# Performance work log

Measured on AMD Instinct MI355X. Metric: run time of the kernel, lower is better.

## Reference

```python
import jax, jax.numpy as jnp
import numpy as np

DIM = 256
NUM_HEADS = 8
HEAD_DIM = DIM // NUM_HEADS


def setup_inputs() -> dict:
    key = jax.random.key(0)
    k1, k2, k3, k4 = jax.random.split(key, 4)
    B, C, H, W = 16, DIM, 64, 64
    x = jax.random.normal(k1, (B, C, H, W), dtype=jnp.float32)
    # 1x1 convs as dense weight matrices [out_ch, in_ch]
    Wqkv = jax.random.normal(k2, (3 * DIM, DIM), dtype=jnp.float32) * (DIM ** -0.5)
    Wproj = jax.random.normal(k3, (DIM, DIM), dtype=jnp.float32) * (DIM ** -0.5)
    bproj = jax.random.normal(k4, (DIM,), dtype=jnp.float32) * 0.01
    return {"x": x, "Wqkv": Wqkv, "Wproj": Wproj, "bproj": bproj}


def reference(x, Wqkv, Wproj, bproj):
    B, C, H, W = x.shape
    N = H * W
    hd = C // NUM_HEADS

    # qkv: 1x1 conv (no bias) == channel matmul
    qkv = jnp.einsum('oc,bchw->bohw', Wqkv, x)  # [B, 3C, H, W]
    q, k, v = jnp.split(qkv, 3, axis=1)

    def to_heads(t):
        # b (h d) x y -> b h (x y) d
        return t.reshape(B, NUM_HEADS, hd, N).transpose(0, 1, 3, 2)

    q, k, v = to_heads(q), to_heads(k), to_heads(v)  # [B, h, N, d]

    # linear attention feature map + per-token normalization over d
    q = jax.nn.elu(q) + 1.0
    k = jax.nn.elu(k) + 1.0
    q = q / jnp.sum(q, axis=-1, keepdims=True)
    k = k / jnp.sum(k, axis=-1, keepdims=True)

    kv = jnp.einsum('bhnd,bhne->bhde', k, v)   # [B, h, d, d]
    out = jnp.einsum('bhnd,bhde->bhne', q, kv)  # [B, h, N, d]

    # b h (x y) d -> b (h d) x y
    out = out.transpose(0, 1, 3, 2).reshape(B, C, H, W)

    # proj: 1x1 conv with bias; drop_path is identity in eval mode
    out = jnp.einsum('oc,bchw->bohw', Wproj, out) + bproj[None, :, None, None]
    return out + x
```

## Files before the change

kernel.cpp:

```cpp
#include <hip/hip_runtime.h>
#include <stdint.h>
#include <stddef.h>

#define DIM   256
#define NH    8
#define HD    32
#define BATCH 16
#define NTOK  4096

typedef __attribute__((ext_vector_type(8))) short short8;
typedef __attribute__((ext_vector_type(4))) float f32x4;

__device__ __forceinline__ unsigned short f2bf(float x){
  unsigned u = __float_as_uint(x);
  u += 0x7fffu + ((u >> 16) & 1u);
  return (unsigned short)(u >> 16);
}
__device__ __forceinline__ float elu1(float v){
  return (v > 0.f) ? (v + 1.f) : __expf(v);
}
__device__ __forceinline__ void gload_lds16(const void* g, void* lds){
  __builtin_amdgcn_global_load_lds(
      (const __attribute__((address_space(1))) unsigned int*)g,
      (__attribute__((address_space(3))) unsigned int*)lds, 16, 0, 0);
}

__global__ __launch_bounds__(256) void k_transpose_x(const float* __restrict__ x,
                                                     unsigned short* __restrict__ xt){
  __shared__ float tile[64][65];
  const int b = blockIdx.z, c0 = blockIdx.y * 64, n0 = blockIdx.x * 64;
  const float* xb = x + (size_t)b * DIM * NTOK;
  const int t = threadIdx.x;
  #pragma unroll
  for (int p = 0; p < 4; p++){
    int idx = t + p * 256;
    int row = idx >> 4;
    int col = (idx & 15) << 2;
    float4 v = *(const float4*)(xb + (size_t)(c0 + row) * NTOK + n0 + col);
    tile[row][col] = v.x; tile[row][col+1] = v.y; tile[row][col+2] = v.z; tile[row][col+3] = v.w;
  }
  __syncthreads();
  unsigned short* xtb = xt + (size_t)b * NTOK * DIM;
  #pragma unroll
  for (int p = 0; p < 4; p++){
    int idx = t + p * 256;
    int nl = idx >> 4;
    int cl = (idx & 15) << 2;
    ushort4 o;
    o.x = f2bf(tile[cl+0][nl]); o.y = f2bf(tile[cl+1][nl]);
    o.z = f2bf(tile[cl+2][nl]); o.w = f2bf(tile[cl+3][nl]);
    *(ushort4*)(xtb + (size_t)(n0 + nl) * DIM + c0 + cl) = o;
  }
}

__global__ __launch_bounds__(256) void k_convert_w(const float* __restrict__ wqkv,
                                                   unsigned short* __restrict__ wq_bf){
  int i = blockIdx.x * 256 + threadIdx.x;
  int row = i >> 6;
  int c4 = (i & 63) * 4;
  int dst;
  if (row < 256)      dst = row;
  else if (row < 512){ int p = (row - 256) >> 6; int s = (row - 256) & 63; dst = 256 + p*128 + s; }
  else               { int p = (row - 512) >> 6; int s = (row - 512) & 63; dst = 256 + p*128 + 64 + s; }
  float4 v = *(const float4*)(wqkv + (size_t)row * DIM + c4);
  ushort4 o = { f2bf(v.x), f2bf(v.y), f2bf(v.z), f2bf(v.w) };
  *(ushort4*)(wq_bf + (size_t)dst * DIM + c4) = o;
}

__global__ __launch_bounds__(256) void k_qkv4(const unsigned short* __restrict__ wbf,
                                              const unsigned short* __restrict__ xt,
                                              unsigned short* __restrict__ qn,
                                              float* __restrict__ kvp){
  __shared__ __align__(16) unsigned short sh[17408];
  unsigned short* As = sh;
  unsigned short* Bs = sh + 8192;
  const int t = threadIdx.x;
  const int w = t >> 6, l = t & 63;
  const int t16 = l & 15, quad = l >> 4;
  const int wm = w >> 1, wn = w & 1;
  const int bid = blockIdx.x;
  const int super = bid / 48;
  const int rem = bid - super * 48;
  const int m = rem >> 3, lx = rem & 7;
  const int g = super * 8 + lx;
  const int nt = g >> 4, b = g & 15;
  const int o0 = m * 128, n0 = nt * 128;
  const unsigned short* A = wbf;
  const unsigned short* B = xt + (size_t)b * NTOK * DIM;

  f32x4 acc[4][4];
  #pragma unroll
  for (int i = 0; i < 4; i++)
    #pragma unroll
    for (int j = 0; j < 4; j++){ acc[i][j][0]=0.f; acc[i][j][1]=0.f; acc[i][j][2]=0.f; acc[i][j][3]=0.f; }

  for (int k0 = 0; k0 < 256; k0 += 64){
    __syncthreads();
    #pragma unroll
    for (int j = 0; j < 4; j++){
      int s = w * 4 + j;
      int tile = s >> 1, kk = s & 1;
      gload_lds16(A + (size_t)(o0 + tile*16 + t16) * DIM + k0 + kk*32 + quad*8, As + s * 512);
      gload_lds16(B + (size_t)(n0 + tile*16 + t16) * DIM + k0 + kk*32 + quad*8, Bs + s * 512);
    }
    __syncthreads();
    #pragma unroll
    for (int kk = 0; kk < 2; kk++){
      short8 a[4], bb[4];
      #pragma unroll
      for (int i = 0; i < 4; i++) a[i]  = *(const short8*)(As + ((wm*4 + i)*2 + kk) * 512 + l * 8);
      #pragma unroll
      for (int j = 0; j < 4; j++) bb[j] = *(const short8*)(Bs + ((wn*4 + j)*2 + kk) * 512 + l * 8);
      #pragma unroll
      for (int i = 0; i < 4; i++)
        #pragma unroll
        for (int j = 0; j < 4; j++)
          acc[i][j] = __builtin_amdgcn_mfma_f32_16x16x32_bf16(a[i], bb[j], acc[i][j], 0, 0, 0);
    }
  }
  __syncthreads();

  const bool isQ = (o0 < 256);
  if (isQ || wm == 0){
    #pragma unroll
    for (int i = 0; i < 4; i++)
      #pragma unroll
      for (int j = 0; j < 4; j++)
        #pragma unroll
        for (int r = 0; r < 4; r++) acc[i][j][r] = elu1(acc[i][j][r]);
    float s[2][4];
    #pragma unroll
    for (int hi = 0; hi < 2; hi++)
      #pragma unroll
      for (int j = 0; j < 4; j++){
        float v = 0.f;
        #pragma unroll
        for (int ii = 0; ii < 2; ii++)
          #pragma unroll
          for (int r = 0; r < 4; r++) v += acc[hi*2 + ii][j][r];
        v += __shfl_xor(v, 16);
        v += __shfl_xor(v, 32);
        s[hi][j] = 1.0f / v;
      }
    #pragma unroll
    for (int i = 0; i < 4; i++)
      #pragma unroll
      for (int j = 0; j < 4; j++){
        float inv = s[i>>1][j];
        #pragma unroll
        for (int r = 0; r < 4; r++) acc[i][j][r] *= inv;
      }
  }

  if (isQ){
    #pragma unroll
    for (int i = 0; i < 4; i++)
      #pragma unroll
      for (int j = 0; j < 4; j++){
        int n_l = wn*64 + j*16 + t16;
        #pragma unroll
        for (int r = 0; r < 4; r++){
          int o_l = wm*64 + i*16 + quad*4 + r;
          sh[n_l*136 + o_l] = f2bf(acc[i][j][r]);
        }
      }
  } else {
    #pragma unroll
    for (int i = 0; i < 4; i++)
      #pragma unroll
      for (int j = 0; j < 4; j++){
        int n_l = wn*64 + j*16 + t16;
        #pragma unroll
        for (int r = 0; r < 4; r++){
          int o_l = wm*64 + i*16 + quad*4 + r;
          sh[o_l*136 + n_l] = f2bf(acc[i][j][r]);
        }
      }
  }
  __syncthreads();

  if (isQ){
    unsigned short* dst = qn + (size_t)b * NTOK * DIM;
    #pragma unroll
    for (int p = 0; p < 8; p++){
      int gg = t + p * 256;
      int n_l = gg >> 4, c = gg & 15;
      uint4 v = *(const uint4*)(sh + n_l*136 + c*8);
      *(uint4*)(dst + (size_t)(n0 + n_l) * DIM + o0 + c*8) = v;
    }
  } else {
    const int p = (o0 >> 7) - 2;
    const int hl = w >> 1, eh = w & 1;
    f32x4 kvacc[2];
    kvacc[0][0]=0.f; kvacc[0][1]=0.f; kvacc[0][2]=0.f; kvacc[0][3]=0.f;
    kvacc[1][0]=0.f; kvacc[1][1]=0.f; kvacc[1][2]=0.f; kvacc[1][3]=0.f;
    const unsigned short* kbase = sh + (hl*32) * 136;
    const unsigned short* vbase = sh + (64 + hl*32 + eh*16) * 136;
    #pragma unroll
    for (int kk = 0; kk < 4; kk++){
      int nn = kk*32 + quad*8;
      short8 bfrag = *(const short8*)(vbase + t16*136 + nn);
      #pragma unroll
      for (int ti = 0; ti < 2; ti++){
        short8 afrag = *(const short8*)(kbase + (ti*16 + t16)*136 + nn);
        kvacc[ti] = __builtin_amdgcn_mfma_f32_16x16x32_bf16(afrag, bfrag, kvacc[ti], 0, 0, 0);
      }
    }
    float* dst = kvp + ((size_t)(b*8 + p*2 + hl) * 32 + nt) * 1024;
    #pragma unroll
    for (int ti = 0; ti < 2; ti++)
      #pragma unroll
      for (int r = 0; r < 4; r++)
        dst[(ti*16 + quad*4 + r)*32 + eh*16 + t16] = kvacc[ti][r];
  }
}

__global__ __launch_bounds__(256) void k_M(const float* __restrict__ kvp,
                                           const float* __restrict__ wproj,
                                           unsigned short* __restrict__ M){
  __shared__ float kvL[1024];
  __shared__ float wpL[8192];
  const int t = threadIdx.x;
  const int h = blockIdx.x, b = blockIdx.y;
  const float* pbase = kvp + (size_t)((b*8 + h)*32) * 1024;
  {
    float4 a = {0.f,0.f,0.f,0.f};
    #pragma unroll
    for (int p = 0; p < 32; p++){
      float4 v = *(const float4*)(pbase + (size_t)p*1024 + t*4);
      a.x += v.x; a.y += v.y; a.z += v.z; a.w += v.w;
    }
    *(float4*)(kvL + t*4) = a;
  }
  #pragma unroll
  for (int p = 0; p < 8; p++){
    int idx = t + p * 256;
    int o = idx >> 3, e4 = idx & 7;
    *(float4*)(wpL + o*32 + e4*4) = *(const float4*)(wproj + (size_t)o * DIM + h*32 + e4*4);
  }
  __syncthreads();
  float wr[32];
  #pragma unroll
  for (int e = 0; e < 32; e++) wr[e] = wpL[t*32 + e];
  unsigned short md[32];
  #pragma unroll
  for (int d = 0; d < 32; d++){
    float a = 0.f;
    #pragma unroll
    for (int e = 0; e < 32; e++) a += wr[e] * kvL[d*32 + e];
    md[d] = f2bf(a);
  }
  unsigned short* dst = M + (size_t)b * 65536 + (size_t)t * DIM + h*32;
  #pragma unroll
  for (int q = 0; q < 4; q++) *(uint4*)(dst + q*8) = *(const uint4*)(md + q*8);
}

__global__ __launch_bounds__(256) void k_out4(const unsigned short* __restrict__ M,
                                              const unsigned short* __restrict__ qn,
                                              const float* __restrict__ x,
                                              const float* __restrict__ bproj,
                                              float* __restrict__ out){
  __shared__ __align__(16) unsigned short As[8192];
  __shared__ __align__(16) unsigned short Bs[8192];
  const int t = threadIdx.x;
  const int w = t >> 6, l = t & 63;
  const int t16 = l & 15, quad = l >> 4;
  const int wm = w >> 1, wn = w & 1;
  const int bid = blockIdx.x;
  const int super = bid >> 4;
  const int rem = bid & 15;
  const int m = rem >> 3, lx = rem & 7;
  const int g = super * 8 + lx;
  const int nt = g >> 4, b = g & 15;
  const int o0 = m * 128, n0 = nt * 128;
  const unsigned short* A = M + (size_t)b * 65536;
  const unsigned short* B = qn + (size_t)b * NTOK * DIM;

  f32x4 acc[4][4];
  #pragma unroll
  for (int i = 0; i < 4; i++)
    #pragma unroll
    for (int j = 0; j < 4; j++){ acc[i][j][0]=0.f; acc[i][j][1]=0.f; acc[i][j][2]=0.f; acc[i][j][3]=0.f; }

  for (int k0 = 0; k0 < 256; k0 += 64){
    __syncthreads();
    #pragma unroll
    for (int j = 0; j < 4; j++){
      int s = w * 4 + j;
      int tile = s >> 1, kk = s & 1;
      gload_lds16(A + (size_t)(o0 + tile*16 + t16) * DIM + k0 + kk*32 + quad*8, As + s * 512);
      gload_lds16(B + (size_t)(n0 + tile*16 + t16) * DIM + k0 + kk*32 + quad*8, Bs + s * 512);
    }
    __syncthreads();
    #pragma unroll
    for (int kk = 0; kk < 2; kk++){
      short8 a[4], bb[4];
      #pragma unroll
      for (int i = 0; i < 4; i++) a[i]  = *(const short8*)(As + ((wm*4 + i)*2 + kk) * 512 + l * 8);
      #pragma unroll
      for (int j = 0; j < 4; j++) bb[j] = *(const short8*)(Bs + ((wn*4 + j)*2 + kk) * 512 + l * 8);
      #pragma unroll
      for (int i = 0; i < 4; i++)
        #pragma unroll
        for (int j = 0; j < 4; j++)
          acc[i][j] = __builtin_amdgcn_mfma_f32_16x16x32_bf16(a[i], bb[j], acc[i][j], 0, 0, 0);
    }
  }

  const float* xb = x + (size_t)b * DIM * NTOK;
  float* ob = out + (size_t)b * DIM * NTOK;
  #pragma unroll
  for (int i = 0; i < 4; i++){
    #pragma unroll
    for (int r = 0; r < 4; r++){
      int o = o0 + wm*64 + i*16 + quad*4 + r;
      float bias = bproj[o];
      #pragma unroll
      for (int j = 0; j < 4; j++){
        int n = n0 + wn*64 + j*16 + t16;
        float v = acc[i][j][r] + bias + xb[(size_t)o * NTOK + n];
        ob[(size_t)o * NTOK + n] = v;
      }
    }
  }
}

extern "C" void kernel_launch(void* const* d_in, const int* in_sizes, int n_in,
                              void* d_out, int out_size, void* d_ws, size_t ws_size,
                              hipStream_t stream){
  const float* x     = (const float*)d_in[0];
  const float* wqkv  = (const float*)d_in[1];
  const float* wproj = (const float*)d_in[2];
  const float* bproj = (const float*)d_in[3];
  float* out = (float*)d_out;
  char* ws = (char*)d_ws;

  unsigned short* xt   = (unsigned short*)(ws);
  unsigned short* qn   = (unsigned short*)(ws + ((size_t)32 << 20));
  float* kvp           = (float*)(ws + ((size_t)64 << 20));
  unsigned short* M    = (unsigned short*)(ws + ((size_t)80 << 20));
  unsigned short* wqbf = (unsigned short*)(ws + ((size_t)82 << 20));

  k_transpose_x<<<dim3(64, 4, 16), 256, 0, stream>>>(x, xt);
  k_convert_w  <<<dim3(192), 256, 0, stream>>>(wqkv, wqbf);
  k_qkv4       <<<dim3(3072), 256, 0, stream>>>(wqbf, xt, qn, kvp);
  k_M          <<<dim3(8, 16), 256, 0, stream>>>(kvp, wproj, M);
  k_out4       <<<dim3(1024), 256, 0, stream>>>(M, qn, x, bproj, out);
}
```

Baseline: 251.5 us.

## Use 512-thread blocks with 8 waves and vectorized epilogues in GEMM kernels

Both the QKV and the output-projection GEMM kernels move from 4 waves to 8 waves per 128x128 tile, so each wave holds half as many accumulators, which lowers register pressure and raises wave occupancy. The output kernel swaps its A/B operands so each thread's accumulator values are contiguous along tokens, which enables float4 loads of x and float4 stores of the output. The Q path now packs its bf16 stores into LDS as ushort4, and the KV partial product is split across 8 waves. The cost is more waves contending for barriers and LDS per tile, with less reuse of each MFMA operand per wave.

```diff
diff --git a/kernel.cpp b/kernel.cpp
--- a/kernel.cpp
+++ b/kernel.cpp
@@ -67,10 +67,10 @@
   *(ushort4*)(wq_bf + (size_t)dst * DIM + c4) = o;
 }
 
-__global__ __launch_bounds__(256) void k_qkv4(const unsigned short* __restrict__ wbf,
-                                              const unsigned short* __restrict__ xt,
-                                              unsigned short* __restrict__ qn,
-                                              float* __restrict__ kvp){
+__global__ __launch_bounds__(512, 4) void k_qkv5(const unsigned short* __restrict__ wbf,
+                                                 const unsigned short* __restrict__ xt,
+                                                 unsigned short* __restrict__ qn,
+                                                 float* __restrict__ kvp){
   __shared__ __align__(16) unsigned short sh[17408];
   unsigned short* As = sh;
   unsigned short* Bs = sh + 8192;
@@ -88,31 +88,34 @@
   const unsigned short* A = wbf;
   const unsigned short* B = xt + (size_t)b * NTOK * DIM;
 
-  f32x4 acc[4][4];
-  #pragma unroll
-  for (int i = 0; i < 4; i++)
+  f32x4 acc[2][4];
+  #pragma unroll
+  for (int i = 0; i < 2; i++)
     #pragma unroll
     for (int j = 0; j < 4; j++){ acc[i][j][0]=0.f; acc[i][j][1]=0.f; acc[i][j][2]=0.f; acc[i][j][3]=0.f; }
 
   for (int k0 = 0; k0 < 256; k0 += 64){
     __syncthreads();
     #pragma unroll
-    for (int j = 0; j < 4; j++){
-      int s = w * 4 + j;
-      int tile = s >> 1, kk = s & 1;
-      gload_lds16(A + (size_t)(o0 + tile*16 + t16) * DIM + k0 + kk*32 + quad*8, As + s * 512);
-      gload_lds16(B + (size_t)(n0 + tile*16 + t16) * DIM + k0 + kk*32 + quad*8, Bs + s * 512);
+    for (int s4 = 0; s4 < 4; s4++){
+      int s = w * 4 + s4;
+      int sl = s & 15;
+      int tile = sl >> 1, kk = sl & 1;
+      const unsigned short* src = (s < 16)
+          ? (A + (size_t)(o0 + tile*16 + t16) * DIM + k0 + kk*32 + quad*8)
+          : (B + (size_t)(n0 + tile*16 + t16) * DIM + k0 + kk*32 + quad*8);
+      gload_lds16(src, sh + s * 512);
     }
     __syncthreads();
     #pragma unroll
     for (int kk = 0; kk < 2; kk++){
-      short8 a[4], bb[4];
-      #pragma unroll
-      for (int i = 0; i < 4; i++) a[i]  = *(const short8*)(As + ((wm*4 + i)*2 + kk) * 512 + l * 8);
+      short8 a[2], bb[4];
+      #pragma unroll
+      for (int i = 0; i < 2; i++) a[i]  = *(const short8*)(As + ((wm*2 + i)*2 + kk) * 512 + l * 8);
       #pragma unroll
       for (int j = 0; j < 4; j++) bb[j] = *(const short8*)(Bs + ((wn*4 + j)*2 + kk) * 512 + l * 8);
       #pragma unroll
-      for (int i = 0; i < 4; i++)
+      for (int i = 0; i < 2; i++)
         #pragma unroll
         for (int j = 0; j < 4; j++)
           acc[i][j] = __builtin_amdgcn_mfma_f32_16x16x32_bf16(a[i], bb[j], acc[i][j], 0, 0, 0);
@@ -121,32 +124,30 @@
   __syncthreads();
 
   const bool isQ = (o0 < 256);
-  if (isQ || wm == 0){
-    #pragma unroll
-    for (int i = 0; i < 4; i++)
+  if (isQ || wm < 2){
+    #pragma unroll
+    for (int i = 0; i < 2; i++)
       #pragma unroll
       for (int j = 0; j < 4; j++)
         #pragma unroll
         for (int r = 0; r < 4; r++) acc[i][j][r] = elu1(acc[i][j][r]);
-    float s[2][4];
-    #pragma unroll
-    for (int hi = 0; hi < 2; hi++)
+    float s[4];
+    #pragma unroll
+    for (int j = 0; j < 4; j++){
+      float v = 0.f;
+      #pragma unroll
+      for (int i = 0; i < 2; i++)
+        #pragma unroll
+        for (int r = 0; r < 4; r++) v += acc[i][j][r];
+      v += __shfl_xor(v, 16);
+      v += __shfl_xor(v, 32);
+      s[j] = 1.0f / v;
+    }
+    #pragma unroll
+    for (int i = 0; i < 2; i++)
       #pragma unroll
       for (int j = 0; j < 4; j++){
-        float v = 0.f;
-        #pragma unroll
-        for (int ii = 0; ii < 2; ii++)
-          #pragma unroll
-          for (int r = 0; r < 4; r++) v += acc[hi*2 + ii][j][r];
-        v += __shfl_xor(v, 16);
-        v += __shfl_xor(v, 32);
-        s[hi][j] = 1.0f / v;
-      }
-    #pragma unroll
-    for (int i = 0; i < 4; i++)
-      #pragma unroll
-      for (int j = 0; j < 4; j++){
-        float inv = s[i>>1][j];
+        float inv = s[j];
         #pragma unroll
         for (int r = 0; r < 4; r++) acc[i][j][r] *= inv;
       }
@@ -154,64 +155,54 @@
 
   if (isQ){
     #pragma unroll
-    for (int i = 0; i < 4; i++)
+    for (int i = 0; i < 2; i++)
       #pragma unroll
       for (int j = 0; j < 4; j++){
         int n_l = wn*64 + j*16 + t16;
-        #pragma unroll
-        for (int r = 0; r < 4; r++){
-          int o_l = wm*64 + i*16 + quad*4 + r;
-          sh[n_l*136 + o_l] = f2bf(acc[i][j][r]);
-        }
+        int o_l0 = wm*32 + i*16 + quad*4;
+        ushort4 pk = { f2bf(acc[i][j][0]), f2bf(acc[i][j][1]),
+                       f2bf(acc[i][j][2]), f2bf(acc[i][j][3]) };
+        *(ushort4*)(sh + n_l*136 + o_l0) = pk;
       }
+    __syncthreads();
+    unsigned short* dst = qn + (size_t)b * NTOK * DIM;
+    #pragma unroll
+    for (int p = 0; p < 4; p++){
+      int gg = t + p * 512;
+      int n_l = gg >> 4, c = gg & 15;
+      uint4 v = *(const uint4*)(sh + n_l*136 + c*8);
+      *(uint4*)(dst + (size_t)(n0 + n_l) * DIM + o0 + c*8) = v;
+    }
   } else {
     #pragma unroll
-    for (int i = 0; i < 4; i++)
+    for (int i = 0; i < 2; i++)
       #pragma unroll
       for (int j = 0; j < 4; j++){
         int n_l = wn*64 + j*16 + t16;
         #pragma unroll
         for (int r = 0; r < 4; r++){
-          int o_l = wm*64 + i*16 + quad*4 + r;
+          int o_l = wm*32 + i*16 + quad*4 + r;
           sh[o_l*136 + n_l] = f2bf(acc[i][j][r]);
         }
       }
-  }
-  __syncthreads();
-
-  if (isQ){
-    unsigned short* dst = qn + (size_t)b * NTOK * DIM;
-    #pragma unroll
-    for (int p = 0; p < 8; p++){
-      int gg = t + p * 256;
-      int n_l = gg >> 4, c = gg & 15;
-      uint4 v = *(const uint4*)(sh + n_l*136 + c*8);
-      *(uint4*)(dst + (size_t)(n0 + n_l) * DIM + o0 + c*8) = v;
-    }
-  } else {
+    __syncthreads();
     const int p = (o0 >> 7) - 2;
-    const int hl = w >> 1, eh = w & 1;
-    f32x4 kvacc[2];
-    kvacc[0][0]=0.f; kvacc[0][1]=0.f; kvacc[0][2]=0.f; kvacc[0][3]=0.f;
-    kvacc[1][0]=0.f; kvacc[1][1]=0.f; kvacc[1][2]=0.f; kvacc[1][3]=0.f;
-    const unsigned short* kbase = sh + (hl*32) * 136;
+    const int hl = w >> 2, dh = (w >> 1) & 1, eh = w & 1;
+    f32x4 kvacc;
+    kvacc[0]=0.f; kvacc[1]=0.f; kvacc[2]=0.f; kvacc[3]=0.f;
+    const unsigned short* kbase = sh + (hl*32 + dh*16) * 136;
     const unsigned short* vbase = sh + (64 + hl*32 + eh*16) * 136;
     #pragma unroll
     for (int kk = 0; kk < 4; kk++){
       int nn = kk*32 + quad*8;
+      short8 afrag = *(const short8*)(kbase + t16*136 + nn);
       short8 bfrag = *(const short8*)(vbase + t16*136 + nn);
-      #pragma unroll
-      for (int ti = 0; ti < 2; ti++){
-        short8 afrag = *(const short8*)(kbase + (ti*16 + t16)*136 + nn);
-        kvacc[ti] = __builtin_amdgcn_mfma_f32_16x16x32_bf16(afrag, bfrag, kvacc[ti], 0, 0, 0);
-      }
+      kvacc = __builtin_amdgcn_mfma_f32_16x16x32_bf16(afrag, bfrag, kvacc, 0, 0, 0);
     }
     float* dst = kvp + ((size_t)(b*8 + p*2 + hl) * 32 + nt) * 1024;
     #pragma unroll
-    for (int ti = 0; ti < 2; ti++)
-      #pragma unroll
-      for (int r = 0; r < 4; r++)
-        dst[(ti*16 + quad*4 + r)*32 + eh*16 + t16] = kvacc[ti][r];
+    for (int r = 0; r < 4; r++)
+      dst[(dh*16 + quad*4 + r)*32 + eh*16 + t16] = kvacc[r];
   }
 }
 
@@ -255,11 +246,11 @@
   for (int q = 0; q < 4; q++) *(uint4*)(dst + q*8) = *(const uint4*)(md + q*8);
 }
 
-__global__ __launch_bounds__(256) void k_out4(const unsigned short* __restrict__ M,
-                                              const unsigned short* __restrict__ qn,
-                                              const float* __restrict__ x,
-                                              const float* __restrict__ bproj,
-                                              float* __restrict__ out){
+__global__ __launch_bounds__(512, 4) void k_out5(const unsigned short* __restrict__ M,
+                                                 const unsigned short* __restrict__ qn,
+                                                 const float* __restrict__ x,
+                                                 const float* __restrict__ bproj,
+                                                 float* __restrict__ out){
   __shared__ __align__(16) unsigned short As[8192];
   __shared__ __align__(16) unsigned short Bs[8192];
   const int t = threadIdx.x;
@@ -273,34 +264,37 @@
   const int g = super * 8 + lx;
   const int nt = g >> 4, b = g & 15;
   const int o0 = m * 128, n0 = nt * 128;
-  const unsigned short* A = M + (size_t)b * 65536;
-  const unsigned short* B = qn + (size_t)b * NTOK * DIM;
-
-  f32x4 acc[4][4];
-  #pragma unroll
-  for (int i = 0; i < 4; i++)
+  const unsigned short* A = qn + (size_t)b * NTOK * DIM;
+  const unsigned short* Bm = M + (size_t)b * 65536;
+
+  f32x4 acc[2][4];
+  #pragma unroll
+  for (int i = 0; i < 2; i++)
     #pragma unroll
     for (int j = 0; j < 4; j++){ acc[i][j][0]=0.f; acc[i][j][1]=0.f; acc[i][j][2]=0.f; acc[i][j][3]=0.f; }
 
   for (int k0 = 0; k0 < 256; k0 += 64){
     __syncthreads();
     #pragma unroll
-    for (int j = 0; j < 4; j++){
-      int s = w * 4 + j;
-      int tile = s >> 1, kk = s & 1;
-      gload_lds16(A + (size_t)(o0 + tile*16 + t16) * DIM + k0 + kk*32 + quad*8, As + s * 512);
-      gload_lds16(B + (size_t)(n0 + tile*16 + t16) * DIM + k0 + kk*32 + quad*8, Bs + s * 512);
+    for (int s4 = 0; s4 < 4; s4++){
+      int s = w * 4 + s4;
+      int sl = s & 15;
+      int tile = sl >> 1, kk = sl & 1;
+      const unsigned short* src = (s < 16)
+          ? (A  + (size_t)(n0 + tile*16 + t16) * DIM + k0 + kk*32 + quad*8)
+          : (Bm + (size_t)(o0 + tile*16 + t16) * DIM + k0 + kk*32 + quad*8);
+      gload_lds16(src, (s < 16) ? (As + sl * 512) : (Bs + sl * 512));
     }
     __syncthreads();
     #pragma unroll
     for (int kk = 0; kk < 2; kk++){
-      short8 a[4], bb[4];
-      #pragma unroll
-      for (int i = 0; i < 4; i++) a[i]  = *(const short8*)(As + ((wm*4 + i)*2 + kk) * 512 + l * 8);
+      short8 a[2], bb[4];
+      #pragma unroll
+      for (int i = 0; i < 2; i++) a[i]  = *(const short8*)(As + ((wm*2 + i)*2 + kk) * 512 + l * 8);
       #pragma unroll
       for (int j = 0; j < 4; j++) bb[j] = *(const short8*)(Bs + ((wn*4 + j)*2 + kk) * 512 + l * 8);
       #pragma unroll
-      for (int i = 0; i < 4; i++)
+      for (int i = 0; i < 2; i++)
         #pragma unroll
         for (int j = 0; j < 4; j++)
           acc[i][j] = __builtin_amdgcn_mfma_f32_16x16x32_bf16(a[i], bb[j], acc[i][j], 0, 0, 0);
@@ -310,17 +304,18 @@
   const float* xb = x + (size_t)b * DIM * NTOK;
   float* ob = out + (size_t)b * DIM * NTOK;
   #pragma unroll
-  for (int i = 0; i < 4; i++){
-    #pragma unroll
-    for (int r = 0; r < 4; r++){
-      int o = o0 + wm*64 + i*16 + quad*4 + r;
-      float bias = bproj[o];
-      #pragma unroll
-      for (int j = 0; j < 4; j++){
-        int n = n0 + wn*64 + j*16 + t16;
-        float v = acc[i][j][r] + bias + xb[(size_t)o * NTOK + n];
-        ob[(size_t)o * NTOK + n] = v;
-      }
+  for (int j = 0; j < 4; j++){
+    int o = o0 + wn*64 + j*16 + t16;
+    float bias = bproj[o];
+    #pragma unroll
+    for (int i = 0; i < 2; i++){
+      int n = n0 + wm*32 + i*16 + quad*4;
+      float4 xv = *(const float4*)(xb + (size_t)o * NTOK + n);
+      float4 res = { acc[i][j][0] + bias + xv.x,
+                     acc[i][j][1] + bias + xv.y,
+                     acc[i][j][2] + bias + xv.z,
+                     acc[i][j][3] + bias + xv.w };
+      *(float4*)(ob + (size_t)o * NTOK + n) = res;
     }
   }
 }
@@ -343,7 +338,7 @@
 
   k_transpose_x<<<dim3(64, 4, 16), 256, 0, stream>>>(x, xt);
   k_convert_w  <<<dim3(192), 256, 0, stream>>>(wqkv, wqbf);
-  k_qkv4       <<<dim3(3072), 256, 0, stream>>>(wqbf, xt, qn, kvp);
+  k_qkv5       <<<dim3(3072), 512, 0, stream>>>(wqbf, xt, qn, kvp);
   k_M          <<<dim3(8, 16), 256, 0, stream>>>(kvp, wproj, M);
-  k_out4       <<<dim3(1024), 256, 0, stream>>>(M, qn, x, bproj, out);
-}
+  k_out5       <<<dim3(1024), 512, 0, stream>>>(M, qn, x, bproj, out);
+}
```

After: 229.9 us. 8.6% less time.
